# Performance work log

Hardware: AMD Instinct MI355X
Metric: run time of the kernel (lower is better)

The kernel has to match this reference:

```python
import jax, jax.numpy as jnp
import numpy as np

CHANNELS = 256
CODEBOOK_SIZE = 8192
UPDATE_SPEED = 0.01
N_TOKENS = 32768


def setup_inputs() -> dict:
    key = jax.random.key(0)
    k1, k2 = jax.random.split(key)
    embeddings = jax.random.normal(k1, (N_TOKENS, CHANNELS), dtype=jnp.float32)
    code_usage = jnp.ones((CODEBOOK_SIZE,), dtype=jnp.float32)
    code_embedding_sum = jax.random.normal(k2, (CODEBOOK_SIZE, CHANNELS), dtype=jnp.float32)
    return {"embeddings": embeddings, "code_usage": code_usage,
            "code_embedding_sum": code_embedding_sum}


def reference(embeddings, code_usage, code_embedding_sum):
    # codebook from EMA statistics: [K, C]
    codebook = code_embedding_sum / jnp.clip(code_usage, 1e-5, None)[:, None]

    # encode: nearest code by Euclidean distance. argmin over codes is
    # invariant under sqrt, so use squared distances (avoids sqrt of [K, N]).
    cb_sq = jnp.sum(codebook * codebook, axis=-1)            # [K]
    x_sq = jnp.sum(embeddings * embeddings, axis=-1)         # [N]
    # d2[k, n] = ||cb_k - x_n||^2
    d2 = cb_sq[:, None] - 2.0 * jnp.einsum('kc,nc->kn', codebook, embeddings) + x_sq[None, :]
    codes = jnp.argmin(d2, axis=0).astype(jnp.int32)         # [N]

    # decode: gather codebook rows
    quantized = jnp.take(codebook, codes, axis=0)            # [N, C]

    # straight-through estimator
    embeddings_q = embeddings + jax.lax.stop_gradient(quantized - embeddings)

    # commitment loss: mse(stop_grad(embeddings_q), embeddings)
    diff = jax.lax.stop_gradient(embeddings_q) - embeddings
    commitment_loss = jnp.mean(diff * diff)

    # EMA updates (training mode, under no_grad in the original)
    n = embeddings.shape[0]
    counts = jax.ops.segment_sum(jnp.ones((n,), dtype=code_usage.dtype),
                                 codes, num_segments=CODEBOOK_SIZE)
    emb_sum = jax.ops.segment_sum(embeddings, codes, num_segments=CODEBOOK_SIZE)
    s = jnp.float32(UPDATE_SPEED)
    new_code_usage = jax.lax.stop_gradient(code_usage * (1.0 - s) + counts * s)
    new_code_embedding_sum = jax.lax.stop_gradient(
        code_embedding_sum * (1.0 - s) + emb_sum * s)

    return codes, embeddings_q, commitment_loss, new_code_usage, new_code_embedding_sum
```

## Files before the change

kernel.cpp:

```cpp
#include <hip/hip_runtime.h>

#define CH 256
#define KC 8192
#define NT 32768

#define TM 128
#define TN 128
#define BK 32
#define YS 2
#define JQ (KC / YS)
#define NSTG ((JQ / TN) * (CH / BK))

typedef _Float16 half4_t __attribute__((ext_vector_type(4)));
typedef _Float16 half8_t __attribute__((ext_vector_type(8)));
typedef float floatx4 __attribute__((ext_vector_type(4)));

typedef __attribute__((address_space(1))) const unsigned int guint_t;
typedef __attribute__((address_space(3))) unsigned int luint_t;

__device__ __forceinline__ int swz(int row, int chunk) {
    return row * BK + ((chunk ^ ((row >> 1) & 3)) << 3);
}

__global__ void k_prep(const float* __restrict__ usage,
                       const float* __restrict__ ces,
                       const float* __restrict__ emb,
                       _Float16* __restrict__ cbh,
                       _Float16* __restrict__ cbl,
                       float* __restrict__ cbsq,
                       _Float16* __restrict__ eh,
                       _Float16* __restrict__ el,
                       int* __restrict__ hist,
                       unsigned long long* __restrict__ packed) {
    int b = blockIdx.x, t = threadIdx.x;
    if (b < KC) {
        float uc = fmaxf(usage[b], 1e-5f);
        float v  = ces[b * CH + t];
        float cb = v / uc;
        _Float16 h = (_Float16)cb;
        cbh[b * CH + t] = h;
        cbl[b * CH + t] = (_Float16)(cb - (float)h);

        float p = cb * cb;
        #pragma unroll
        for (int off = 32; off; off >>= 1) p += __shfl_down(p, off);
        __shared__ float ps[4];
        int lane = t & 63, w = t >> 6;
        if (lane == 0) ps[w] = p;
        __syncthreads();
        if (t == 0) cbsq[b] = ps[0] + ps[1] + ps[2] + ps[3];
        if (t == 1) hist[b] = 0;
        int gid = b * CH + t;
        if (gid < NT) packed[gid] = 0xFFFFFFFFFFFFFFFFull;
    } else {
        int i = (b - KC) * 256 + t;
        float4 v = ((const float4*)emb)[i];
        float va[4] = {v.x, v.y, v.z, v.w};
        half4_t h, l;
        #pragma unroll
        for (int q = 0; q < 4; ++q) {
            _Float16 hh = (_Float16)va[q];
            h[q] = hh;
            l[q] = (_Float16)(va[q] - (float)hh);
        }
        ((half4_t*)eh)[i] = h;
        ((half4_t*)el)[i] = l;
    }
}

__launch_bounds__(256, 2)
__global__ void k_argmin(const _Float16* __restrict__ eh,
                         const _Float16* __restrict__ el,
                         const _Float16* __restrict__ cbh,
                         const _Float16* __restrict__ cbl,
                         const float* __restrict__ cbsq,
                         unsigned long long* __restrict__ packed) {
    __shared__ __align__(16) _Float16 sm[2][4][TM * BK];
    __shared__ float cand_v[2][TM];
    __shared__ int   cand_i[2][TM];

    const int t    = threadIdx.x;
    const int lane = t & 63;
    const int wave = t >> 6;
    const int wx   = wave & 1;
    const int wy   = wave >> 1;
    const int lr   = lane & 15;
    const int koq  = lane >> 4;

    const int id  = blockIdx.x;
    const int xcd = id & 7;
    const int n0  = ((id >> 3) * 4 + (xcd & 3)) * TM;
    const int jq  = (xcd >> 2) * JQ;

    const _Float16* dsrc = (wave == 0) ? eh : (wave == 1) ? el
                         : (wave == 2) ? cbh : cbl;
    const int qsw   = (lane & 3) ^ ((lane >> 3) & 3);
    const int lrow  = lane >> 2;

    float minv[16];
    int   mini[16];
    #pragma unroll
    for (int e = 0; e < 16; ++e) { minv[e] = 3.402823466e38f; mini[e] = 0; }

    floatx4 acc[4][4];
    #pragma unroll
    for (int mf = 0; mf < 4; ++mf)
        #pragma unroll
        for (int nf = 0; nf < 4; ++nf)
            acc[mf][nf] = (floatx4){0.f, 0.f, 0.f, 0.f};

    auto dma = [&](int buf, int sg) {
        const int c0 = (sg & 7) * BK;
        const int jb = jq + (sg >> 3) * TN;
        const int rb = (wave < 2) ? n0 : jb;
        const _Float16* gbase = dsrc + (size_t)(rb + lrow) * CH + c0 + qsw * 8;
        #pragma unroll
        for (int i = 0; i < 8; ++i) {
            const _Float16* g = gbase + (size_t)(i * 16) * CH;
            __builtin_amdgcn_global_load_lds(
                (guint_t*)g, (luint_t*)&sm[buf][wave][i * 512], 16, 0, 0);
        }
    };

    dma(0, 0);
    asm volatile("s_waitcnt vmcnt(0)" ::: "memory");
    __builtin_amdgcn_s_barrier();
    __builtin_amdgcn_sched_barrier(0);

    float csq[4] = {0.f, 0.f, 0.f, 0.f};

    #pragma unroll 1
    for (int s = 0; s < NSTG; ++s) {
        const int cur = s & 1;

        if ((s & 7) == 0) {
            int jbase = jq + (s >> 3) * TN;
            #pragma unroll
            for (int nf = 0; nf < 4; ++nf)
                csq[nf] = cbsq[jbase + wx * 64 + nf * 16 + lr];
        }

        if (s + 1 < NSTG) dma(cur ^ 1, s + 1);

        half8_t fah[4], fal[4];
        #pragma unroll
        for (int mf = 0; mf < 4; ++mf) {
            int off = swz(wy * 64 + mf * 16 + lr, koq);
            fah[mf] = *(const half8_t*)&sm[cur][0][off];
            fal[mf] = *(const half8_t*)&sm[cur][1][off];
        }
        __builtin_amdgcn_s_setprio(1);
        #pragma unroll
        for (int nf = 0; nf < 4; ++nf) {
            int offb = swz(wx * 64 + nf * 16 + lr, koq);
            half8_t fbh = *(const half8_t*)&sm[cur][2][offb];
            half8_t fbl = *(const half8_t*)&sm[cur][3][offb];
            #pragma unroll
            for (int mf = 0; mf < 4; ++mf) {
                acc[mf][nf] = __builtin_amdgcn_mfma_f32_16x16x32_f16(
                    fah[mf], fbh, acc[mf][nf], 0, 0, 0);
                acc[mf][nf] = __builtin_amdgcn_mfma_f32_16x16x32_f16(
                    fah[mf], fbl, acc[mf][nf], 0, 0, 0);
                acc[mf][nf] = __builtin_amdgcn_mfma_f32_16x16x32_f16(
                    fal[mf], fbh, acc[mf][nf], 0, 0, 0);
            }
        }
        __builtin_amdgcn_s_setprio(0);

        if ((s & 7) == 7) {
            int jbase = jq + (s >> 3) * TN;
            #pragma unroll
            for (int nf = 0; nf < 4; ++nf) {
                int j = jbase + wx * 64 + nf * 16 + lr;
                float sq = csq[nf];
                #pragma unroll
                for (int mf = 0; mf < 4; ++mf) {
                    floatx4 a = acc[mf][nf];
                    #pragma unroll
                    for (int r = 0; r < 4; ++r) {
                        float sc = sq - 2.0f * a[r];
                        int e = mf * 4 + r;
                        if (sc < minv[e]) { minv[e] = sc; mini[e] = j; }
                    }
                    acc[mf][nf] = (floatx4){0.f, 0.f, 0.f, 0.f};
                }
            }
        }

        asm volatile("s_waitcnt vmcnt(0)" ::: "memory");
        __builtin_amdgcn_sched_barrier(0);
        __builtin_amdgcn_s_barrier();
        __builtin_amdgcn_sched_barrier(0);
    }

    #pragma unroll
    for (int e = 0; e < 16; ++e) {
        float v = minv[e];
        int   x = mini[e];
        #pragma unroll
        for (int m = 1; m <= 8; m <<= 1) {
            float ov = __shfl_xor(v, m, 64);
            int   ox = __shfl_xor(x, m, 64);
            if (ov < v || (ov == v && ox < x)) { v = ov; x = ox; }
        }
        if (lr == 0) {
            int row = wy * 64 + (e >> 2) * 16 + (lane >> 4) * 4 + (e & 3);
            cand_v[wx][row] = v;
            cand_i[wx][row] = x;
        }
    }
    __syncthreads();

    if (t < TM) {
        float v0 = cand_v[0][t]; int i0 = cand_i[0][t];
        float v1 = cand_v[1][t]; int i1 = cand_i[1][t];
        if (v1 < v0 || (v1 == v0 && i1 < i0)) { v0 = v1; i0 = i1; }
        unsigned sb = __float_as_uint(v0);
        sb = (sb & 0x80000000u) ? ~sb : (sb | 0x80000000u);
        unsigned long long key = ((unsigned long long)sb << 32) | (unsigned)i0;
        atomicMin(&packed[n0 + t], key);
    }
}

__global__ void k_gather(const float* __restrict__ emb,
                         const float* __restrict__ ces,
                         const float* __restrict__ usage,
                         const unsigned long long* __restrict__ packed,
                         float* __restrict__ out_eq,
                         float* __restrict__ codes_f,
                         int* __restrict__ hist,
                         float* __restrict__ partials) {
    int t = threadIdx.x;
    int wave = t >> 6, lane = t & 63;
    int n = blockIdx.x * 4 + wave;
    int k = (int)(packed[n] & 0xFFFFFFFFull);
    float uc = fmaxf(usage[k], 1e-5f);
    int c = lane * 4;

    float4 e = *(const float4*)&emb[(size_t)n * CH + c];
    float4 v = *(const float4*)&ces[(size_t)k * CH + c];
    float ea[4] = {e.x, e.y, e.z, e.w};
    float va[4] = {v.x, v.y, v.z, v.w};
    float eqa[4];
    float p = 0.0f;
    #pragma unroll
    for (int q = 0; q < 4; ++q) {
        float cb = va[q] / uc;
        float eq = ea[q] + (cb - ea[q]);
        eqa[q] = eq;
        float d = eq - ea[q];
        p += d * d;
    }
    *(float4*)&out_eq[(size_t)n * CH + c] =
        (float4){eqa[0], eqa[1], eqa[2], eqa[3]};

    #pragma unroll
    for (int off = 32; off; off >>= 1) p += __shfl_down(p, off);
    __shared__ float ps[4];
    if (lane == 0) {
        ps[wave] = p;
        codes_f[n] = (float)k;
        atomicAdd(&hist[k], 1);
    }
    __syncthreads();
    if (t == 0) partials[blockIdx.x] = ps[0] + ps[1] + ps[2] + ps[3];
}

__global__ void k_scan(const int* __restrict__ hist,
                       int* __restrict__ offs,
                       int* __restrict__ cursor) {
    __shared__ int bs[256];
    int t = threadIdx.x;
    int base = t * 32;
    int loc[32];
    int s = 0;
    #pragma unroll
    for (int i = 0; i < 32; ++i) { loc[i] = s; s += hist[base + i]; }
    int mysum = s;
    bs[t] = s;
    __syncthreads();
    for (int off = 1; off < 256; off <<= 1) {
        int v = (t >= off) ? bs[t - off] : 0;
        __syncthreads();
        bs[t] += v;
        __syncthreads();
    }
    int excl = bs[t] - mysum;
    #pragma unroll
    for (int i = 0; i < 32; ++i) {
        int o = excl + loc[i];
        offs[base + i]   = o;
        cursor[base + i] = o;
    }
}

__global__ void k_scatter(const unsigned long long* __restrict__ packed,
                          int* __restrict__ cursor,
                          int* __restrict__ bucket) {
    int n = blockIdx.x * 256 + threadIdx.x;
    int k = (int)(packed[n] & 0xFFFFFFFFull);
    int pos = atomicAdd(&cursor[k], 1);
    bucket[pos] = n;
}

__global__ void k_ema(const float* __restrict__ emb,
                      const float* __restrict__ ces,
                      const float* __restrict__ usage,
                      const int* __restrict__ hist,
                      const int* __restrict__ offs,
                      const int* __restrict__ bucket,
                      float* __restrict__ out_ces,
                      float* __restrict__ out_usage) {
    const float s = 0.01f;
    const float oms = 1.0f - s;
    int k = blockIdx.x, t = threadIdx.x;
    int start = offs[k], cnt = hist[k];
    float sum = 0.0f;
    #pragma unroll 2
    for (int i = 0; i < cnt; ++i) {
        int n = bucket[start + i];
        sum += emb[(size_t)n * CH + t];
    }
    out_ces[(size_t)k * CH + t] = oms * ces[(size_t)k * CH + t] + s * sum;
    if (t == 0) out_usage[k] = oms * usage[k] + s * (float)cnt;
}

__global__ void k_final(const float* __restrict__ partials,
                        float* __restrict__ out_loss) {
    int t = threadIdx.x;
    float p = 0.0f;
    for (int i = t; i < NT / 4; i += 256) p += partials[i];
    #pragma unroll
    for (int off = 32; off; off >>= 1) p += __shfl_down(p, off);
    __shared__ float ps[4];
    if ((t & 63) == 0) ps[t >> 6] = p;
    __syncthreads();
    if (t == 0)
        out_loss[0] = (ps[0] + ps[1] + ps[2] + ps[3]) * (1.0f / 8388608.0f);
}

extern "C" void kernel_launch(void* const* d_in, const int* in_sizes, int n_in,
                              void* d_out, int out_size, void* d_ws, size_t ws_size,
                              hipStream_t stream) {
    const float* emb   = (const float*)d_in[0];
    const float* usage = (const float*)d_in[1];
    const float* ces   = (const float*)d_in[2];

    float* out      = (float*)d_out;
    float* o_codes  = out;
    float* o_eq     = out + NT;
    float* o_loss   = o_eq + (size_t)NT * CH;
    float* o_usage  = o_loss + 1;
    float* o_ces    = o_usage + KC;

    unsigned long long* packed = (unsigned long long*)d_ws;
    float* cbsq     = (float*)(packed + NT);
    float* partials = cbsq + KC;
    int* hist   = (int*)(partials + NT / 4);
    int* offs   = hist + KC;
    int* cursor = offs + KC;
    int* bucket = cursor + KC;
    _Float16* eh  = (_Float16*)(bucket + NT);
    _Float16* el  = eh + (size_t)NT * CH;
    _Float16* cbh = el + (size_t)NT * CH;
    _Float16* cbl = cbh + (size_t)KC * CH;

    k_prep<<<KC + NT * CH / 1024, 256, 0, stream>>>(
        usage, ces, emb, cbh, cbl, cbsq, eh, el, hist, packed);
    k_argmin<<<(NT / TM) * YS, 256, 0, stream>>>(eh, el, cbh, cbl, cbsq,
                                                 packed);
    k_gather<<<NT / 4, 256, 0, stream>>>(emb, ces, usage, packed, o_eq,
                                         o_codes, hist, partials);
    k_scan<<<1, 256, 0, stream>>>(hist, offs, cursor);
    k_scatter<<<NT / 256, 256, 0, stream>>>(packed, cursor, bucket);
    k_ema<<<KC, 256, 0, stream>>>(emb, ces, usage, hist, offs, bucket,
                                  o_ces, o_usage);
    k_final<<<1, 256, 0, stream>>>(partials, o_loss);
}
```

Measured before the change: 675.2 us.

## Keep full embedding tile resident in LDS and sweep the entire codebook per block

The argmin kernel now uses 512-thread blocks that load the block's whole 128-token hi/lo fp16 embedding tile (all 256 channels) into LDS once, and stream only codebook tiles through a double buffer. Each block covers the whole codebook instead of half, so the 64-bit atomicMin merge and the packed-key initialisation in the prep kernel go away, replaced by a plain store. The cost is 160KB of LDS per block, which limits occupancy to one block per CU, and half as many blocks (256) in the grid. The XCD-aware block remapping is also dropped.

```diff
diff --git a/kernel.cpp b/kernel.cpp
--- a/kernel.cpp
+++ b/kernel.cpp
@@ -7,9 +7,7 @@
 #define TM 128
 #define TN 128
 #define BK 32
-#define YS 2
-#define JQ (KC / YS)
-#define NSTG ((JQ / TN) * (CH / BK))
+#define NSTG ((KC / TN) * (CH / BK))
 
 typedef _Float16 half4_t __attribute__((ext_vector_type(4)));
 typedef _Float16 half8_t __attribute__((ext_vector_type(8)));
@@ -30,8 +28,7 @@
                        float* __restrict__ cbsq,
                        _Float16* __restrict__ eh,
                        _Float16* __restrict__ el,
-                       int* __restrict__ hist,
-                       unsigned long long* __restrict__ packed) {
+                       int* __restrict__ hist) {
     int b = blockIdx.x, t = threadIdx.x;
     if (b < KC) {
         float uc = fmaxf(usage[b], 1e-5f);
@@ -50,8 +47,6 @@
         __syncthreads();
         if (t == 0) cbsq[b] = ps[0] + ps[1] + ps[2] + ps[3];
         if (t == 1) hist[b] = 0;
-        int gid = b * CH + t;
-        if (gid < NT) packed[gid] = 0xFFFFFFFFFFFFFFFFull;
     } else {
         int i = (b - KC) * 256 + t;
         float4 v = ((const float4*)emb)[i];
@@ -68,93 +63,109 @@
     }
 }
 
-__launch_bounds__(256, 2)
+__launch_bounds__(512, 1)
 __global__ void k_argmin(const _Float16* __restrict__ eh,
                          const _Float16* __restrict__ el,
                          const _Float16* __restrict__ cbh,
                          const _Float16* __restrict__ cbl,
                          const float* __restrict__ cbsq,
                          unsigned long long* __restrict__ packed) {
-    __shared__ __align__(16) _Float16 sm[2][4][TM * BK];
-    __shared__ float cand_v[2][TM];
-    __shared__ int   cand_i[2][TM];
+    __shared__ __align__(16) unsigned char smraw[163840];
+    _Float16* smA = (_Float16*)smraw;
+    _Float16* smB = (_Float16*)(smraw + 131072);
 
     const int t    = threadIdx.x;
     const int lane = t & 63;
     const int wave = t >> 6;
-    const int wx   = wave & 1;
-    const int wy   = wave >> 1;
+    const int wx   = wave & 3;
+    const int wy   = wave >> 2;
     const int lr   = lane & 15;
     const int koq  = lane >> 4;
 
-    const int id  = blockIdx.x;
-    const int xcd = id & 7;
-    const int n0  = ((id >> 3) * 4 + (xcd & 3)) * TM;
-    const int jq  = (xcd >> 2) * JQ;
-
-    const _Float16* dsrc = (wave == 0) ? eh : (wave == 1) ? el
-                         : (wave == 2) ? cbh : cbl;
-    const int qsw   = (lane & 3) ^ ((lane >> 3) & 3);
-    const int lrow  = lane >> 2;
+    const int n0 = blockIdx.x * TM;
+
+    const int qsw  = (lane & 3) ^ ((lane >> 3) & 3);
+    const int lrow = lane >> 2;
+
+    const int hl = wave >> 2;
+    const _Float16* asrc = hl ? el : eh;
+    const _Float16* bsrc = hl ? cbl : cbh;
 
     float minv[16];
     int   mini[16];
     #pragma unroll
     for (int e = 0; e < 16; ++e) { minv[e] = 3.402823466e38f; mini[e] = 0; }
 
-    floatx4 acc[4][4];
+    floatx4 acc[4][2];
     #pragma unroll
     for (int mf = 0; mf < 4; ++mf)
         #pragma unroll
-        for (int nf = 0; nf < 4; ++nf)
+        for (int nf = 0; nf < 2; ++nf)
             acc[mf][nf] = (floatx4){0.f, 0.f, 0.f, 0.f};
 
-    auto dma = [&](int buf, int sg) {
+    {
+        const int ccb = (wave & 3) * 2;
+        #pragma unroll
+        for (int d = 0; d < 2; ++d) {
+            const int cc = ccb + d;
+            const _Float16* g0 = asrc + (size_t)(n0 + lrow) * CH + cc * BK
+                               + qsw * 8;
+            #pragma unroll
+            for (int i = 0; i < 8; ++i) {
+                __builtin_amdgcn_global_load_lds(
+                    (guint_t*)(g0 + (size_t)(i * 16) * CH),
+                    (luint_t*)&smA[hl * 32768 + cc * 4096 + i * 512], 16, 0, 0);
+            }
+        }
+    }
+
+    auto dmaB = [&](int buf, int sg) {
         const int c0 = (sg & 7) * BK;
-        const int jb = jq + (sg >> 3) * TN;
-        const int rb = (wave < 2) ? n0 : jb;
-        const _Float16* gbase = dsrc + (size_t)(rb + lrow) * CH + c0 + qsw * 8;
-        #pragma unroll
-        for (int i = 0; i < 8; ++i) {
-            const _Float16* g = gbase + (size_t)(i * 16) * CH;
+        const int jb = (sg >> 3) * TN + wx * 32;
+        const _Float16* g0 = bsrc + (size_t)(jb + lrow) * CH + c0 + qsw * 8;
+        #pragma unroll
+        for (int i = 0; i < 2; ++i) {
             __builtin_amdgcn_global_load_lds(
-                (guint_t*)g, (luint_t*)&sm[buf][wave][i * 512], 16, 0, 0);
+                (guint_t*)(g0 + (size_t)(i * 16) * CH),
+                (luint_t*)&smB[buf * 8192 + hl * 4096 + wx * 1024 + i * 512],
+                16, 0, 0);
         }
     };
 
-    dma(0, 0);
+    dmaB(0, 0);
     asm volatile("s_waitcnt vmcnt(0)" ::: "memory");
     __builtin_amdgcn_s_barrier();
     __builtin_amdgcn_sched_barrier(0);
 
-    float csq[4] = {0.f, 0.f, 0.f, 0.f};
+    float csq[2] = {0.f, 0.f};
 
     #pragma unroll 1
     for (int s = 0; s < NSTG; ++s) {
         const int cur = s & 1;
+        const int cc  = s & 7;
 
         if ((s & 7) == 0) {
-            int jbase = jq + (s >> 3) * TN;
+            int jbase = (s >> 3) * TN;
             #pragma unroll
-            for (int nf = 0; nf < 4; ++nf)
-                csq[nf] = cbsq[jbase + wx * 64 + nf * 16 + lr];
-        }
-
-        if (s + 1 < NSTG) dma(cur ^ 1, s + 1);
+            for (int nf = 0; nf < 2; ++nf)
+                csq[nf] = cbsq[jbase + wx * 32 + nf * 16 + lr];
+        }
+
+        if (s + 1 < NSTG) dmaB(cur ^ 1, s + 1);
 
         half8_t fah[4], fal[4];
         #pragma unroll
         for (int mf = 0; mf < 4; ++mf) {
-            int off = swz(wy * 64 + mf * 16 + lr, koq);
-            fah[mf] = *(const half8_t*)&sm[cur][0][off];
-            fal[mf] = *(const half8_t*)&sm[cur][1][off];
+            int off = cc * 4096 + swz(wy * 64 + mf * 16 + lr, koq);
+            fah[mf] = *(const half8_t*)&smA[off];
+            fal[mf] = *(const half8_t*)&smA[32768 + off];
         }
         __builtin_amdgcn_s_setprio(1);
         #pragma unroll
-        for (int nf = 0; nf < 4; ++nf) {
-            int offb = swz(wx * 64 + nf * 16 + lr, koq);
-            half8_t fbh = *(const half8_t*)&sm[cur][2][offb];
-            half8_t fbl = *(const half8_t*)&sm[cur][3][offb];
+        for (int nf = 0; nf < 2; ++nf) {
+            int offb = cur * 8192 + swz(wx * 32 + nf * 16 + lr, koq);
+            half8_t fbh = *(const half8_t*)&smB[offb];
+            half8_t fbl = *(const half8_t*)&smB[4096 + offb];
             #pragma unroll
             for (int mf = 0; mf < 4; ++mf) {
                 acc[mf][nf] = __builtin_amdgcn_mfma_f32_16x16x32_f16(
@@ -168,10 +179,10 @@
         __builtin_amdgcn_s_setprio(0);
 
         if ((s & 7) == 7) {
-            int jbase = jq + (s >> 3) * TN;
+            int jbase = (s >> 3) * TN;
             #pragma unroll
-            for (int nf = 0; nf < 4; ++nf) {
-                int j = jbase + wx * 64 + nf * 16 + lr;
+            for (int nf = 0; nf < 2; ++nf) {
+                int j = jbase + wx * 32 + nf * 16 + lr;
                 float sq = csq[nf];
                 #pragma unroll
                 for (int mf = 0; mf < 4; ++mf) {
@@ -193,6 +204,9 @@
         __builtin_amdgcn_sched_barrier(0);
     }
 
+    float* cand_v = (float*)(smraw + 131072);
+    int*   cand_i = (int*)(smraw + 131072 + 4 * TM * 4);
+
     #pragma unroll
     for (int e = 0; e < 16; ++e) {
         float v = minv[e];
@@ -205,20 +219,22 @@
         }
         if (lr == 0) {
             int row = wy * 64 + (e >> 2) * 16 + (lane >> 4) * 4 + (e & 3);
-            cand_v[wx][row] = v;
-            cand_i[wx][row] = x;
+            cand_v[wx * TM + row] = v;
+            cand_i[wx * TM + row] = x;
         }
     }
     __syncthreads();
 
     if (t < TM) {
-        float v0 = cand_v[0][t]; int i0 = cand_i[0][t];
-        float v1 = cand_v[1][t]; int i1 = cand_i[1][t];
-        if (v1 < v0 || (v1 == v0 && i1 < i0)) { v0 = v1; i0 = i1; }
+        float v0 = cand_v[t];          int i0 = cand_i[t];
+        #pragma unroll
+        for (int q = 1; q < 4; ++q) {
+            float v1 = cand_v[q * TM + t]; int i1 = cand_i[q * TM + t];
+            if (v1 < v0 || (v1 == v0 && i1 < i0)) { v0 = v1; i0 = i1; }
+        }
         unsigned sb = __float_as_uint(v0);
         sb = (sb & 0x80000000u) ? ~sb : (sb | 0x80000000u);
-        unsigned long long key = ((unsigned long long)sb << 32) | (unsigned)i0;
-        atomicMin(&packed[n0 + t], key);
+        packed[n0 + t] = ((unsigned long long)sb << 32) | (unsigned)i0;
     }
 }
 
@@ -366,9 +382,8 @@
     _Float16* cbl = cbh + (size_t)KC * CH;
 
     k_prep<<<KC + NT * CH / 1024, 256, 0, stream>>>(
-        usage, ces, emb, cbh, cbl, cbsq, eh, el, hist, packed);
-    k_argmin<<<(NT / TM) * YS, 256, 0, stream>>>(eh, el, cbh, cbl, cbsq,
-                                                 packed);
+        usage, ces, emb, cbh, cbl, cbsq, eh, el, hist);
+    k_argmin<<<NT / TM, 512, 0, stream>>>(eh, el, cbh, cbl, cbsq, packed);
     k_gather<<<NT / 4, 256, 0, stream>>>(emb, ces, usage, packed, o_eq,
                                          o_codes, hist, partials);
     k_scan<<<1, 256, 0, stream>>>(hist, offs, cursor);
```

Measured after the change: 595.2 us. 11.9% less time.
